# Optimization experiments

Measured on AMD Instinct MI355X. Metric: run time of the kernel, lower is better.

## Reference

```python
import jax, jax.numpy as jnp
import numpy as np

# ---- constants from module defaults ----
IMG, PS, STRIDE, C_IN = 224, 16, 8, 1
NP1D = (IMG - PS) // STRIDE + 1          # 27
NUM_PATCHES = NP1D * NP1D                # 729
EMBED = 64
N_INPUT = NUM_PATCHES * EMBED            # 46656
N_HIDDEN = 1000                          # d_model
N_RNN = 100
N_STEPS = 5
BETA, THR = 0.8, 0.5
BETA_R, THR_R = 0.95, 1.0
LM_SPN = 0.0058
ALPHA = 2.0  # snntorch ATan surrogate default

@jax.custom_vjp
def spike(x):
    return (x > 0).astype(x.dtype)

def _spike_fwd(x):
    return spike(x), x

def _spike_bwd(x, g):
    # snntorch ATan surrogate gradient
    return (g * (ALPHA / 2.0) / (1.0 + (jnp.pi / 2.0 * ALPHA * x) ** 2),)

spike.defvjp(_spike_fwd, _spike_bwd)

def extract_patches(x):
    # x: [B, C, H, W] -> [B, num_patches, C*PS*PS] matching torch unfold+permute+flatten
    B, C, H, W = x.shape
    idx = (jnp.arange(NP1D)[:, None] * STRIDE + jnp.arange(PS)).reshape(-1)  # [NP1D*PS]
    t = x[:, :, idx, :].reshape(B, C, NP1D, PS, W)
    t = t[..., idx].reshape(B, C, NP1D, PS, NP1D, PS)
    t = t.transpose(0, 2, 4, 1, 3, 5)  # [B, nh, nw, C, ph, pw]
    return t.reshape(B, NUM_PATCHES, C * PS * PS)

def setup_inputs() -> dict:
    key = jax.random.key(0)
    ks = jax.random.split(key, 12)
    def lin(k, fi, fo):
        kw, kb = jax.random.split(k)
        s = 1.0 / np.sqrt(fi)
        return (jax.random.uniform(kw, (fi, fo), jnp.float32, -s, s),
                jax.random.uniform(kb, (fo,), jnp.float32, -s, s))
    W_pe, b_pe = lin(ks[0], C_IN * PS * PS, EMBED)
    pos_embed = 0.02 * jax.random.normal(ks[1], (1, NUM_PATCHES, EMBED), jnp.float32)
    W1, b1 = lin(ks[2], N_INPUT, N_HIDDEN)
    W2, b2 = lin(ks[3], N_HIDDEN, N_HIDDEN)
    W3, b3 = lin(ks[4], N_HIDDEN, N_HIDDEN)
    WR, bR = lin(ks[5], N_HIDDEN, N_RNN)
    Vw, Vb = lin(ks[6], N_RNN, N_RNN)      # RLeaky recurrent linear
    Wq, bq = lin(ks[7], N_RNN, N_HIDDEN)
    Wk, bk = lin(ks[8], N_HIDDEN, N_HIDDEN)
    Wv, bv = lin(ks[9], N_HIDDEN, N_HIDDEN)
    Wo, bo = lin(ks[10], N_HIDDEN, 1)       # cross_last=True -> output_proj to 1
    data = jax.random.normal(ks[11], (32, C_IN, IMG, IMG), jnp.float32)
    return {"data": data, "W_pe": W_pe, "b_pe": b_pe, "pos_embed": pos_embed,
            "W1": W1, "b1": b1, "W2": W2, "b2": b2, "W3": W3, "b3": b3,
            "WR": WR, "bR": bR, "Vw": Vw, "Vb": Vb,
            "Wq": Wq, "bq": bq, "Wk": Wk, "bk": bk, "Wv": Wv, "bv": bv,
            "Wo": Wo, "bo": bo}

def _forward(data, W_pe, b_pe, pos_embed, W1, b1, W2, b2, W3, b3,
             WR, bR, Vw, Vb, Wq, bq, Wk, bk, Wv, bv, Wo, bo):
    B = data.shape[0]
    patches = extract_patches(data)                      # [B, 729, 256]
    x = patches @ W_pe + b_pe + pos_embed               # [B, 729, 64]
    x_flat = x.reshape(B, -1)                            # [B, 46656]
    cur1 = x_flat @ W1 + b1                              # constant across steps
    scale = jnp.sqrt(jnp.asarray(N_HIDDEN, jnp.float32))  # head_dim = d_model (1 head)

    def leaky(mem, cur, beta=BETA, thr=THR):
        reset = jax.lax.stop_gradient(spike(mem - thr))
        mem = beta * mem + cur - reset * thr
        return mem, spike(mem - thr)

    def step(carry, t):
        mem1, mem2, mem3, spk_r, mem_r, mem_out, total, prev, reg = carry
        # layers[:2] call -- first Leaky1 update
        mem1, spk1 = leaky(mem1, cur1)
        # layers[:7] call -- Leaky1 state updated a SECOND time (same x_flat)
        mem1, spk1b = leaky(mem1, cur1)
        mem2, spk2 = leaky(mem2, spk1b @ W2 + b2)
        mem3, spk3 = leaky(mem3, spk2 @ W3 + b3)  # Dropout is identity in eval
        total = total + spk1.mean() + spk3.mean()
        # RLeaky (beta=0.95, threshold=1.0, subtract reset, recurrent linear)
        rlin = spk1 @ WR + bR
        reset_r = jax.lax.stop_gradient(spike(mem_r - THR_R))
        mem_r = BETA_R * mem_r + rlin + spk_r @ Vw + Vb - reset_r * THR_R
        spk_r = spike(mem_r - THR_R)
        total = total + spk_r.mean()
        # cross-attention: feature dim acts as the sequence dim (seq=1 in view)
        q = spk_r @ Wq + bq                               # [B, 1000]
        k = spk3 @ Wk + bk                                # [B, 1000]
        v = spk3 @ Wv + bv                                # [B, 1000]
        probs = jax.nn.softmax(q[:, :, None] * k[:, None, :] / scale, axis=-1)  # [B,1000,1000]
        att = jnp.einsum('bij,bj->bi', probs, v) @ Wo + bo  # [B, 1]
        mem_out, spk_out = leaky(mem_out, att)
        mem_out = jax.lax.stop_gradient(mem_out)          # .detach() in source
        total = total + spk_out.mean()
        reg = reg + LM_SPN * total + jnp.where(t > 0, LM_SPN * jnp.abs(total - prev), 0.0)
        return (mem1, mem2, mem3, spk_r, mem_r, mem_out, total, total, reg), spk_out

    z = jnp.float32(0.0)
    init = (jnp.zeros((B, N_HIDDEN)), jnp.zeros((B, N_HIDDEN)), jnp.zeros((B, N_HIDDEN)),
            jnp.zeros((B, N_RNN)), jnp.zeros((B, N_RNN)), jnp.zeros((B, 1)), z, z, z)
    carry, spk_rec = jax.lax.scan(step, init, jnp.arange(N_STEPS))
    out = spk_rec.sum(0)[:, 0] / N_STEPS                  # [B]
    reg_norm = carry[-1] / N_STEPS
    return out, reg_norm

def reference(data, W_pe, b_pe, pos_embed, W1, b1, W2, b2, W3, b3,
              WR, bR, Vw, Vb, Wq, bq, Wk, bk, Wv, bv, Wo, bo):
    return _forward(data, W_pe, b_pe, pos_embed, W1, b1, W2, b2, W3, b3,
                    WR, bR, Vw, Vb, Wq, bq, Wk, bk, Wv, bv, Wo, bo)
```

## Files before the change

kernel.cpp:

```cpp
#include <hip/hip_runtime.h>

#define OFF_X     0
#define OFF_CUR1  1492992
#define OFF_MEM1  1524992
#define OFF_MEM2  1556992
#define OFF_MEM3  1588992
#define OFF_MEMR  1844992
#define OFF_SPKR  1848192
#define OFF_MEMO  1851392
#define OFF_PATT  1851424
#define OFF_CNT   1851680
#define OFF_OACC  1851700
#define OFF_SC    1851732
#define OFF_TICK  1851736
#define OFF_PART  1851744
#define OFF_PG2   OFF_PART
#define OFF_PG3   (OFF_PART + 800000)
#define OFF_PKK   (OFF_PART + 1600000)
#define OFF_PVV   (OFF_PART + 2400000)
#define OFF_M2B   (OFF_PART + 3200000)
#define OFF_M3B   (OFF_PART + 3232000)
#define OFF_M1B   (OFF_PART + 3264000)
#define OFF_SPK1  (OFF_PART + 3296000)
#define OFF_MRB   (OFF_PART + 3328000)
#define OFF_SRB   (OFF_PART + 3331200)

static constexpr float kBETA  = 0.8f;
static constexpr float kTHR   = 0.5f;
static constexpr float kBETAR = 0.95f;
static constexpr float kTHRR  = 1.0f;
static constexpr float kLM    = 0.0058f;

__global__ void k_init(float* ws) {
    int idx = blockIdx.x * 256 + threadIdx.x;
    if (idx < 96000) {
        ws[OFF_MEM1 + idx] = 0.f;
    } else {
        int j = idx - 96000;
        if (j < 6752) ws[OFF_MEMR + j] = 0.f;
    }
}

__global__ __launch_bounds__(64) void k_patch(
    const float* __restrict__ data, const float* __restrict__ Wpe,
    const float* __restrict__ bpe, const float* __restrict__ pos,
    float* __restrict__ xf)
{
    int b = blockIdx.x, pr = blockIdx.y;
    int tid = threadIdx.x;
    const float* db = data + (size_t)b * 50176 + pr * 1792;
    float bb = bpe[tid];
    float acc[27];
    #pragma unroll
    for (int pc = 0; pc < 27; ++pc)
        acc[pc] = bb + pos[(pr * 27 + pc) * 64 + tid];
    #pragma unroll 2
    for (int c = 0; c < 256; ++c) {
        float w = Wpe[c * 64 + tid];
        const float* row = db + (c >> 4) * 224 + (c & 15);
        #pragma unroll
        for (int pc = 0; pc < 27; ++pc)
            acc[pc] = fmaf(row[pc * 8], w, acc[pc]);
    }
    size_t obase = (size_t)b * 46656 + (size_t)pr * 27 * 64 + tid;
    #pragma unroll
    for (int pc = 0; pc < 27; ++pc)
        xf[obase + (size_t)pc * 64] = acc[pc];
}

__global__ __launch_bounds__(256) void k_gemm1_part(
    const float* __restrict__ xf, const float* __restrict__ W1,
    float* __restrict__ part, int tpc)
{
    int chunk = blockIdx.x;
    int hg = blockIdx.y;
    int t0 = chunk * tpc;
    int t1 = t0 + tpc; if (t1 > 729) t1 = 729;
    int tid = threadIdx.x;
    __shared__ float xs[2048];
    float acc[32][2];
    #pragma unroll
    for (int b = 0; b < 32; ++b) { acc[b][0] = 0.f; acc[b][1] = 0.f; }

    const int hbase = hg * 500;
    const bool ok1 = (tid + 256) < 500;
    const int h0 = hbase + tid;
    const int h1 = hbase + (ok1 ? tid + 256 : 0);
    for (int tt = t0; tt < t1; ++tt) {
        int i0 = tt * 64;
        __syncthreads();
        for (int l = tid; l < 2048; l += 256)
            xs[l] = xf[(size_t)(l >> 6) * 46656 + i0 + (l & 63)];
        __syncthreads();
        for (int ii4 = 0; ii4 < 16; ++ii4) {
            int i = i0 + ii4 * 4;
            const float* c0 = W1 + (size_t)i * 1000 + h0;
            const float* c1 = W1 + (size_t)i * 1000 + h1;
            float w0a = c0[0], w1a = c0[1000], w2a = c0[2000], w3a = c0[3000];
            float w0b = ok1 ? c1[0]    : 0.f;
            float w1b = ok1 ? c1[1000] : 0.f;
            float w2b = ok1 ? c1[2000] : 0.f;
            float w3b = ok1 ? c1[3000] : 0.f;
            #pragma unroll
            for (int b = 0; b < 32; ++b) {
                float4 xv = *reinterpret_cast<const float4*>(&xs[b * 64 + ii4 * 4]);
                float a0 = acc[b][0], a1 = acc[b][1];
                a0 = fmaf(xv.x, w0a, a0);  a1 = fmaf(xv.x, w0b, a1);
                a0 = fmaf(xv.y, w1a, a0);  a1 = fmaf(xv.y, w1b, a1);
                a0 = fmaf(xv.z, w2a, a0);  a1 = fmaf(xv.z, w2b, a1);
                a0 = fmaf(xv.w, w3a, a0);  a1 = fmaf(xv.w, w3b, a1);
                acc[b][0] = a0; acc[b][1] = a1;
            }
        }
    }
    float* pc = part + (size_t)chunk * 32000 + hbase;
    #pragma unroll
    for (int b = 0; b < 32; ++b) {
        pc[b * 1000 + tid] = acc[b][0];
        if (ok1) pc[b * 1000 + tid + 256] = acc[b][1];
    }
}

__global__ void k_gemm1_reduce(const float* __restrict__ part,
                               const float* __restrict__ b1,
                               float* __restrict__ cur1, int nchunk)
{
    int idx = blockIdx.x * 128 + threadIdx.x;
    if (idx >= 32000) return;
    int h = idx % 1000;
    float a0 = b1[h], a1 = 0.f, a2 = 0.f, a3 = 0.f;
    int c = 0;
    for (; c + 4 <= nchunk; c += 4) {
        a0 += part[(size_t)c * 32000 + idx];
        a1 += part[(size_t)(c + 1) * 32000 + idx];
        a2 += part[(size_t)(c + 2) * 32000 + idx];
        a3 += part[(size_t)(c + 3) * 32000 + idx];
    }
    for (; c < nchunk; ++c) a0 += part[(size_t)c * 32000 + idx];
    cur1[idx] = (a0 + a1) + (a2 + a3);
}

__global__ __launch_bounds__(256) void k_gsp(
    const float* __restrict__ cur1, const float* __restrict__ mem1_old,
    float* __restrict__ mem1_new, float* __restrict__ spk1_out,
    const float* __restrict__ W, float* __restrict__ part, float* cnt0)
{
    int hb = blockIdx.x, kc = blockIdx.y, bg = blockIdx.z;
    int tid = threadIdx.x;
    int j0 = kc * 40;
    __shared__ __align__(16) float al[320];
    __shared__ float redg[8 * 128];
    __shared__ float csum[4];
    float localc = 0.f;
    for (int e = tid; e < 320; e += 256) {
        int jj = e % 40, bi = e / 40;
        int idx = (bg * 8 + bi) * 1000 + j0 + jj;
        float m = mem1_old[idx], c = cur1[idx];
        float r1 = (m - kTHR > 0.f) ? kTHR : 0.f;
        float ma = __fsub_rn(__fadd_rn(__fmul_rn(kBETA, m), c), r1);
        float s1 = (ma - kTHR > 0.f) ? 1.f : 0.f;
        float r2 = __fmul_rn(s1, kTHR);
        float mb = __fsub_rn(__fadd_rn(__fmul_rn(kBETA, ma), c), r2);
        float s1b = (mb - kTHR > 0.f) ? 1.f : 0.f;
        al[jj * 8 + bi] = s1b;
        if (hb == 0) { mem1_new[idx] = mb; spk1_out[idx] = s1; localc += s1; }
    }
    for (int off = 32; off; off >>= 1) localc += __shfl_down(localc, off, 64);
    if ((tid & 63) == 0) csum[tid >> 6] = localc;
    __syncthreads();
    if (hb == 0 && tid == 0) {
        float tot = csum[0] + csum[1] + csum[2] + csum[3];
        if (tot != 0.f) atomicAdd(cnt0, tot);
    }
    int ks = tid >> 7, hh = tid & 127;
    float acc[8];
    #pragma unroll
    for (int b = 0; b < 8; ++b) acc[b] = 0.f;
    if (hh < 125) {
        int h = hb * 125 + hh;
        const float* Wp = W + (size_t)(j0 + ks * 20) * 1000 + h;
        const float4* abase = reinterpret_cast<const float4*>(&al[ks * 20 * 8]);
        #pragma unroll 4
        for (int jj = 0; jj < 20; ++jj) {
            float w = Wp[(size_t)jj * 1000];
            const float4* a4 = abase + jj * 2;
            #pragma unroll
            for (int q = 0; q < 2; ++q) {
                float4 av = a4[q];
                acc[q * 4 + 0] = fmaf(av.x, w, acc[q * 4 + 0]);
                acc[q * 4 + 1] = fmaf(av.y, w, acc[q * 4 + 1]);
                acc[q * 4 + 2] = fmaf(av.z, w, acc[q * 4 + 2]);
                acc[q * 4 + 3] = fmaf(av.w, w, acc[q * 4 + 3]);
            }
        }
    }
    if (ks == 1 && hh < 125) {
        #pragma unroll
        for (int b = 0; b < 8; ++b) redg[b * 128 + hh] = acc[b];
    }
    __syncthreads();
    if (ks == 0 && hh < 125) {
        int h = hb * 125 + hh;
        float* pp = part + (size_t)kc * 32000 + (size_t)(bg * 8) * 1000 + h;
        #pragma unroll
        for (int b = 0; b < 8; ++b) pp[(size_t)b * 1000] = acc[b] + redg[b * 128 + hh];
    }
}

template <bool COUNT>
__global__ __launch_bounds__(256) void k_gspred(
    const float* __restrict__ pin, const float* __restrict__ bias,
    const float* __restrict__ mem_old, float* __restrict__ mem_new,
    const float* __restrict__ W, float* __restrict__ pout, float* cnt)
{
    int hs = blockIdx.x, kc = blockIdx.y, bg = blockIdx.z;
    int tid = threadIdx.x;
    int j0 = kc * 40;
    __shared__ __align__(16) float al[320];
    __shared__ float redg[8 * 128];
    __shared__ float csum[4];
    float localc = 0.f;
    for (int e = tid; e < 320; e += 256) {
        int jj = e % 40, bi = e / 40;
        int idx = (bg * 8 + bi) * 1000 + j0 + jj;
        float a = bias[j0 + jj];
        #pragma unroll 5
        for (int c = 0; c < 25; ++c) a += pin[(size_t)c * 32000 + idx];
        float m = mem_old[idx];
        float r = (m - kTHR > 0.f) ? kTHR : 0.f;
        float mn = __fsub_rn(__fadd_rn(__fmul_rn(kBETA, m), a), r);
        float s = (mn - kTHR > 0.f) ? 1.f : 0.f;
        al[jj * 8 + bi] = s;
        if (hs == 0) { mem_new[idx] = mn; localc += s; }
    }
    if (COUNT) {
        for (int off = 32; off; off >>= 1) localc += __shfl_down(localc, off, 64);
        if ((tid & 63) == 0) csum[tid >> 6] = localc;
    }
    __syncthreads();
    if (COUNT && tid == 0 && hs == 0) {
        float tot = csum[0] + csum[1] + csum[2] + csum[3];
        if (tot != 0.f) atomicAdd(cnt, tot);
    }
    int ks = tid >> 7, hh = tid & 127;
    float acc[8];
    #pragma unroll
    for (int b = 0; b < 8; ++b) acc[b] = 0.f;
    if (hh < 125) {
        int h = hs * 125 + hh;
        const float* Wp = W + (size_t)(j0 + ks * 20) * 1000 + h;
        const float4* abase = reinterpret_cast<const float4*>(&al[ks * 20 * 8]);
        #pragma unroll 4
        for (int jj = 0; jj < 20; ++jj) {
            float w = Wp[(size_t)jj * 1000];
            const float4* a4 = abase + jj * 2;
            #pragma unroll
            for (int q = 0; q < 2; ++q) {
                float4 av = a4[q];
                acc[q * 4 + 0] = fmaf(av.x, w, acc[q * 4 + 0]);
                acc[q * 4 + 1] = fmaf(av.y, w, acc[q * 4 + 1]);
                acc[q * 4 + 2] = fmaf(av.z, w, acc[q * 4 + 2]);
                acc[q * 4 + 3] = fmaf(av.w, w, acc[q * 4 + 3]);
            }
        }
    }
    if (ks == 1 && hh < 125) {
        #pragma unroll
        for (int b = 0; b < 8; ++b) redg[b * 128 + hh] = acc[b];
    }
    __syncthreads();
    if (ks == 0 && hh < 125) {
        int h = hs * 125 + hh;
        float* pp = pout + (size_t)kc * 32000 + (size_t)(bg * 8) * 1000 + h;
        #pragma unroll
        for (int b = 0; b < 8; ++b) pp[(size_t)b * 1000] = acc[b] + redg[b * 128 + hh];
    }
}

__global__ __launch_bounds__(256) void k_gspred_kv(
    const float* __restrict__ pin, const float* __restrict__ bias,
    const float* __restrict__ mem_old, float* __restrict__ mem_new,
    const float* __restrict__ Wk, const float* __restrict__ Wv,
    float* __restrict__ pk, float* __restrict__ pv, float* cnt)
{
    int hs = blockIdx.x, kc = blockIdx.y, bg = blockIdx.z;
    int tid = threadIdx.x;
    int j0 = kc * 40;
    __shared__ __align__(16) float al[320];
    __shared__ float redk[8 * 128];
    __shared__ float redv[8 * 128];
    __shared__ float csum[4];
    float localc = 0.f;
    for (int e = tid; e < 320; e += 256) {
        int jj = e % 40, bi = e / 40;
        int idx = (bg * 8 + bi) * 1000 + j0 + jj;
        float a = bias[j0 + jj];
        #pragma unroll 5
        for (int c = 0; c < 25; ++c) a += pin[(size_t)c * 32000 + idx];
        float m = mem_old[idx];
        float r = (m - kTHR > 0.f) ? kTHR : 0.f;
        float mn = __fsub_rn(__fadd_rn(__fmul_rn(kBETA, m), a), r);
        float s = (mn - kTHR > 0.f) ? 1.f : 0.f;
        al[jj * 8 + bi] = s;
        if (hs == 0) { mem_new[idx] = mn; localc += s; }
    }
    for (int off = 32; off; off >>= 1) localc += __shfl_down(localc, off, 64);
    if ((tid & 63) == 0) csum[tid >> 6] = localc;
    __syncthreads();
    if (tid == 0 && hs == 0) {
        float tot = csum[0] + csum[1] + csum[2] + csum[3];
        if (tot != 0.f) atomicAdd(cnt, tot);
    }
    int ks = tid >> 7, hh = tid & 127;
    float ak[8], av2[8];
    #pragma unroll
    for (int b = 0; b < 8; ++b) { ak[b] = 0.f; av2[b] = 0.f; }
    if (hh < 125) {
        int h = hs * 125 + hh;
        const float* wkp = Wk + (size_t)(j0 + ks * 20) * 1000 + h;
        const float* wvp = Wv + (size_t)(j0 + ks * 20) * 1000 + h;
        const float4* abase = reinterpret_cast<const float4*>(&al[ks * 20 * 8]);
        #pragma unroll 4
        for (int jj = 0; jj < 20; ++jj) {
            float wk = wkp[(size_t)jj * 1000];
            float wv = wvp[(size_t)jj * 1000];
            const float4* a4 = abase + jj * 2;
            #pragma unroll
            for (int q = 0; q < 2; ++q) {
                float4 av = a4[q];
                ak[q * 4 + 0] = fmaf(av.x, wk, ak[q * 4 + 0]);
                ak[q * 4 + 1] = fmaf(av.y, wk, ak[q * 4 + 1]);
                ak[q * 4 + 2] = fmaf(av.z, wk, ak[q * 4 + 2]);
                ak[q * 4 + 3] = fmaf(av.w, wk, ak[q * 4 + 3]);
                av2[q * 4 + 0] = fmaf(av.x, wv, av2[q * 4 + 0]);
                av2[q * 4 + 1] = fmaf(av.y, wv, av2[q * 4 + 1]);
                av2[q * 4 + 2] = fmaf(av.z, wv, av2[q * 4 + 2]);
                av2[q * 4 + 3] = fmaf(av.w, wv, av2[q * 4 + 3]);
            }
        }
    }
    if (ks == 1 && hh < 125) {
        #pragma unroll
        for (int b = 0; b < 8; ++b) { redk[b * 128 + hh] = ak[b]; redv[b * 128 + hh] = av2[b]; }
    }
    __syncthreads();
    if (ks == 0 && hh < 125) {
        int h = hs * 125 + hh;
        float* ppk = pk + (size_t)kc * 32000 + (size_t)(bg * 8) * 1000 + h;
        float* ppv = pv + (size_t)kc * 32000 + (size_t)(bg * 8) * 1000 + h;
        #pragma unroll
        for (int b = 0; b < 8; ++b) {
            ppk[(size_t)b * 1000] = ak[b] + redk[b * 128 + hh];
            ppv[(size_t)b * 1000] = av2[b] + redv[b * 128 + hh];
        }
    }
}

__global__ __launch_bounds__(512) void k_attnred(
    const float* __restrict__ pkk, const float* __restrict__ pvv,
    const float* __restrict__ bk, const float* __restrict__ bv,
    const float* __restrict__ spk1, const float* __restrict__ WR,
    const float* __restrict__ bR, const float* __restrict__ Vw,
    const float* __restrict__ Vb,
    const float* __restrict__ memr_old, float* __restrict__ memr_new,
    const float* __restrict__ spkr_old, float* __restrict__ spkr_new,
    const float* __restrict__ Wq, const float* __restrict__ bq,
    const float* __restrict__ Wo, const float* __restrict__ bo,
    float* __restrict__ patt, float* __restrict__ memo,
    float* __restrict__ oacc, const float* __restrict__ cnt,
    float* __restrict__ sc, float* __restrict__ dout,
    unsigned int* __restrict__ tick, float* cnt2, int t)
{
    int it = blockIdx.x, b = blockIdx.y;
    int tid = threadIdx.x;
    __shared__ float kk[1000], vv[1000];
    __shared__ float sr[100];
    __shared__ float s1l[1000];
    __shared__ float red2[512];
    __shared__ float red[512];
    __shared__ float pden[512], pnum[512];
    __shared__ int isLast;

    for (int l = tid; l < 1000; l += 512) s1l[l] = spk1[b * 1000 + l];
    if (tid < 100) sr[tid] = spkr_old[b * 100 + tid];
    __syncthreads();
    int ks4 = tid >> 7, hh4 = tid & 127;
    float p = 0.f;
    if (hh4 < 100) {
        const float* wp = WR + (size_t)(ks4 * 250) * 100 + hh4;
        int j0r = ks4 * 250;
        #pragma unroll 5
        for (int j = 0; j < 250; ++j) p = fmaf(s1l[j0r + j], wp[(size_t)j * 100], p);
    }
    red2[ks4 * 128 + hh4] = p;
    __syncthreads();
    float snew = 0.f;
    if (tid < 100) {
        float acc = bR[tid] + ((red2[tid] + red2[128 + tid]) + (red2[256 + tid] + red2[384 + tid]));
        float rec = 0.f;
        for (int j = 0; j < 100; ++j) rec = fmaf(sr[j], Vw[j * 100 + tid], rec);
        float m = memr_old[b * 100 + tid];
        float r = (m - kTHRR > 0.f) ? kTHRR : 0.f;
        float mn = __fsub_rn(__fadd_rn(__fadd_rn(__fadd_rn(__fmul_rn(kBETAR, m), acc), rec), Vb[tid]), r);
        snew = (mn - kTHRR > 0.f) ? 1.f : 0.f;
        if (it == 0) { memr_new[b * 100 + tid] = mn; spkr_new[b * 100 + tid] = snew; }
    }
    if (it == 0) {
        unsigned long long mskr = __ballot(snew > 0.5f);
        if ((tid & 63) == 0) {
            int pc2 = __popcll(mskr);
            if (pc2) atomicAdd(cnt2, (float)pc2);
        }
    }
    __syncthreads();
    if (tid < 100) sr[tid] = snew;
    __syncthreads();

    float pmax = -3.4e38f, pmin = 3.4e38f;
    for (int h = tid; h < 1000; h += 512) {
        int idx = b * 1000 + h;
        float ak = bk[h], av = bv[h];
        #pragma unroll 5
        for (int c = 0; c < 25; ++c) {
            ak += pkk[(size_t)c * 32000 + idx];
            av += pvv[(size_t)c * 32000 + idx];
        }
        kk[h] = ak; vv[h] = av;
        pmax = fmaxf(pmax, ak);
        pmin = fminf(pmin, ak);
    }
    red[tid] = pmax;
    __syncthreads();
    for (int s2 = 256; s2 > 0; s2 >>= 1) {
        if (tid < s2) red[tid] = fmaxf(red[tid], red[tid + s2]);
        __syncthreads();
    }
    float kmax = red[0];
    __syncthreads();
    red[tid] = pmin;
    __syncthreads();
    for (int s2 = 256; s2 > 0; s2 >>= 1) {
        if (tid < s2) red[tid] = fminf(red[tid], red[tid + s2]);
        __syncthreads();
    }
    float kmin = red[0];
    __syncthreads();

    int quarter = tid >> 7, lane = tid & 127;
    float den = 0.f, num = 0.f;
    if (lane < 125) {
        int i = it * 125 + lane;
        float qi = bq[i];
        for (int j = 0; j < 100; ++j) qi = fmaf(sr[j], Wq[j * 1000 + i], qi);
        float qs = qi / 31.62277660168379f;
        float m = (qs >= 0.f) ? qs * kmax : qs * kmin;
        int jb = quarter * 250;
        for (int j = 0; j < 250; ++j) {
            float e = __expf(fmaf(qs, kk[jb + j], -m));
            den += e;
            num = fmaf(e, vv[jb + j], num);
        }
    }
    pden[tid] = den; pnum[tid] = num;
    __syncthreads();
    float pw = 0.f;
    if (tid < 125) {
        float dsum = (pden[tid] + pden[tid + 128]) + (pden[tid + 256] + pden[tid + 384]);
        float nsum = (pnum[tid] + pnum[tid + 128]) + (pnum[tid + 256] + pnum[tid + 384]);
        pw = (nsum / dsum) * Wo[it * 125 + tid];
    }
    red[tid] = (tid < 125) ? pw : 0.f;
    __syncthreads();
    for (int s2 = 256; s2 > 0; s2 >>= 1) {
        if (tid < s2) red[tid] += red[tid + s2];
        __syncthreads();
    }
    if (tid == 0) patt[b * 8 + it] = red[0];
    __syncthreads();
    if (tid == 0) {
        __threadfence();
        unsigned r = atomicAdd(tick, 1u);
        isLast = (r == 255u) ? 1 : 0;
    }
    __syncthreads();
    if (isLast && tid < 64) {
        __threadfence();
        float s = 0.f;
        if (tid < 32) {
            float a = bo[0];
            for (int itx = 0; itx < 8; ++itx) a += patt[tid * 8 + itx];
            float m = memo[tid];
            float r = (m - kTHR > 0.f) ? kTHR : 0.f;
            float mn = __fsub_rn(__fadd_rn(__fmul_rn(kBETA, m), a), r);
            memo[tid] = mn;
            s = (mn - kTHR > 0.f) ? 1.f : 0.f;
            float oa = oacc[tid] + s;
            oacc[tid] = oa;
            if (t == 4) dout[tid] = oa / 5.0f;
        }
        unsigned long long msk = __ballot(s > 0.5f);
        float co = (float)__popcll(msk);
        if (tid == 0) {
            float total = sc[0];
            float prev = total;
            total = __fadd_rn(total, __fdiv_rn(cnt[0], 32000.f));
            total = __fadd_rn(total, __fdiv_rn(cnt[1], 32000.f));
            total = __fadd_rn(total, __fdiv_rn(cnt[2], 3200.f));
            total = __fadd_rn(total, __fdiv_rn(co, 32.f));
            float reg = sc[1];
            reg = __fadd_rn(reg, __fmul_rn(kLM, total));
            if (t > 0) reg = __fadd_rn(reg, __fmul_rn(kLM, fabsf(__fsub_rn(total, prev))));
            sc[0] = total; sc[1] = reg;
            if (t == 4) dout[32] = reg / 5.0f;
        }
    }
}

extern "C" void kernel_launch(void* const* d_in, const int* in_sizes, int n_in,
                              void* d_out, int out_size, void* d_ws, size_t ws_size,
                              hipStream_t stream)
{
    const float* data = (const float*)d_in[0];
    const float* Wpe  = (const float*)d_in[1];
    const float* bpe  = (const float*)d_in[2];
    const float* pos  = (const float*)d_in[3];
    const float* W1   = (const float*)d_in[4];
    const float* b1   = (const float*)d_in[5];
    const float* W2   = (const float*)d_in[6];
    const float* b2   = (const float*)d_in[7];
    const float* W3   = (const float*)d_in[8];
    const float* b3   = (const float*)d_in[9];
    const float* WR   = (const float*)d_in[10];
    const float* bR   = (const float*)d_in[11];
    const float* Vw   = (const float*)d_in[12];
    const float* Vb   = (const float*)d_in[13];
    const float* Wq   = (const float*)d_in[14];
    const float* bq   = (const float*)d_in[15];
    const float* Wk   = (const float*)d_in[16];
    const float* bk   = (const float*)d_in[17];
    const float* Wv   = (const float*)d_in[18];
    const float* bv   = (const float*)d_in[19];
    const float* Wo   = (const float*)d_in[20];
    const float* bo   = (const float*)d_in[21];

    float* ws = (float*)d_ws;
    float* dout = (float*)d_out;

    float* xf    = ws + OFF_X;
    float* cur1  = ws + OFF_CUR1;
    float* mem1a = ws + OFF_MEM1;
    float* mem2a = ws + OFF_MEM2;
    float* mem3a = ws + OFF_MEM3;
    float* memra = ws + OFF_MEMR;
    float* spkra = ws + OFF_SPKR;
    float* memo  = ws + OFF_MEMO;
    float* patt  = ws + OFF_PATT;
    float* cntb  = ws + OFF_CNT;
    float* oacc  = ws + OFF_OACC;
    float* sc    = ws + OFF_SC;
    unsigned int* tick = (unsigned int*)(ws + OFF_TICK);
    float* part  = ws + OFF_PART;
    float* pg2   = ws + OFF_PG2;
    float* pg3   = ws + OFF_PG3;
    float* pkk   = ws + OFF_PKK;
    float* pvv   = ws + OFF_PVV;
    float* mem2b = ws + OFF_M2B;
    float* mem3b = ws + OFF_M3B;
    float* mem1b = ws + OFF_M1B;
    float* spk1  = ws + OFF_SPK1;
    float* memrb = ws + OFF_MRB;
    float* spkrb = ws + OFF_SRB;

    size_t ws_f = ws_size / 4;
    size_t avail = (ws_f > OFF_PART) ? (ws_f - OFF_PART) : 0;
    long nchunk_l = (long)(avail / 32000);
    int nchunk = (nchunk_l > 365) ? 365 : (int)nchunk_l;
    if (nchunk < 1) nchunk = 1;
    int tpc = (729 + nchunk - 1) / nchunk;
    nchunk = (729 + tpc - 1) / tpc;

    k_init<<<402, 256, 0, stream>>>(ws);
    k_patch<<<dim3(32, 27), 64, 0, stream>>>(data, Wpe, bpe, pos, xf);
    k_gemm1_part<<<dim3(nchunk, 2), 256, 0, stream>>>(xf, W1, part, tpc);
    k_gemm1_reduce<<<250, 128, 0, stream>>>(part, b1, cur1, nchunk);

    for (int t = 0; t < 5; ++t) {
        float* cnt = cntb + t * 4;
        float* m1o = (t & 1) ? mem1b : mem1a;
        float* m1n = (t & 1) ? mem1a : mem1b;
        float* m2o = (t & 1) ? mem2b : mem2a;
        float* m2n = (t & 1) ? mem2a : mem2b;
        float* m3o = (t & 1) ? mem3b : mem3a;
        float* m3n = (t & 1) ? mem3a : mem3b;
        float* mro = (t & 1) ? memrb : memra;
        float* mrn = (t & 1) ? memra : memrb;
        float* sro = (t & 1) ? spkrb : spkra;
        float* srn = (t & 1) ? spkra : spkrb;

        k_gsp<<<dim3(8, 25, 4), 256, 0, stream>>>(
            cur1, m1o, m1n, spk1, W2, pg2, cnt + 0);
        k_gspred<false><<<dim3(8, 25, 4), 256, 0, stream>>>(
            pg2, b2, m2o, m2n, W3, pg3, nullptr);
        k_gspred_kv<<<dim3(8, 25, 4), 256, 0, stream>>>(
            pg3, b3, m3o, m3n, Wk, Wv, pkk, pvv, cnt + 1);
        k_attnred<<<dim3(8, 32), 512, 0, stream>>>(
            pkk, pvv, bk, bv, spk1, WR, bR, Vw, Vb,
            mro, mrn, sro, srn, Wq, bq, Wo, bo,
            patt, memo, oacc, cnt, sc, dout, tick + t, cnt + 2, t);
    }
    (void)in_sizes; (void)n_in; (void)out_size;
}
```

Baseline: 517.7 us.

## Halve batch per block in spiking GEMVs, widen reductions, use wave shuffles

The per-step spiking GEMV kernels now process 4 batch rows per block instead of 8, doubling the grid's z-dimension to put more blocks in flight. The gemm1 reduce kernel unrolls 8 accumulators. The chunk cap for gemm1 partials rises from 365 to 729, so partials can be split further when workspace allows. The attention kernel replaces shared-memory tree reductions with wave shuffles plus a small cross-wave combine. Together these aim to raise occupancy and cut synchronisation, at the cost of re-reading each weight twice as often and possibly more partial-sum traffic.

```diff
diff --git a/kernel.cpp b/kernel.cpp
--- a/kernel.cpp
+++ b/kernel.cpp
@@ -129,15 +129,20 @@
     if (idx >= 32000) return;
     int h = idx % 1000;
     float a0 = b1[h], a1 = 0.f, a2 = 0.f, a3 = 0.f;
+    float a4 = 0.f, a5 = 0.f, a6 = 0.f, a7 = 0.f;
     int c = 0;
-    for (; c + 4 <= nchunk; c += 4) {
+    for (; c + 8 <= nchunk; c += 8) {
         a0 += part[(size_t)c * 32000 + idx];
         a1 += part[(size_t)(c + 1) * 32000 + idx];
         a2 += part[(size_t)(c + 2) * 32000 + idx];
         a3 += part[(size_t)(c + 3) * 32000 + idx];
+        a4 += part[(size_t)(c + 4) * 32000 + idx];
+        a5 += part[(size_t)(c + 5) * 32000 + idx];
+        a6 += part[(size_t)(c + 6) * 32000 + idx];
+        a7 += part[(size_t)(c + 7) * 32000 + idx];
     }
     for (; c < nchunk; ++c) a0 += part[(size_t)c * 32000 + idx];
-    cur1[idx] = (a0 + a1) + (a2 + a3);
+    cur1[idx] = ((a0 + a1) + (a2 + a3)) + ((a4 + a5) + (a6 + a7));
 }
 
 __global__ __launch_bounds__(256) void k_gsp(
@@ -148,13 +153,13 @@
     int hb = blockIdx.x, kc = blockIdx.y, bg = blockIdx.z;
     int tid = threadIdx.x;
     int j0 = kc * 40;
-    __shared__ __align__(16) float al[320];
-    __shared__ float redg[8 * 128];
+    __shared__ __align__(16) float al[160];
+    __shared__ float redg[4 * 128];
     __shared__ float csum[4];
     float localc = 0.f;
-    for (int e = tid; e < 320; e += 256) {
-        int jj = e % 40, bi = e / 40;
-        int idx = (bg * 8 + bi) * 1000 + j0 + jj;
+    if (tid < 160) {
+        int jj = tid % 40, bi = tid / 40;
+        int idx = (bg * 4 + bi) * 1000 + j0 + jj;
         float m = mem1_old[idx], c = cur1[idx];
         float r1 = (m - kTHR > 0.f) ? kTHR : 0.f;
         float ma = __fsub_rn(__fadd_rn(__fmul_rn(kBETA, m), c), r1);
@@ -162,8 +167,8 @@
         float r2 = __fmul_rn(s1, kTHR);
         float mb = __fsub_rn(__fadd_rn(__fmul_rn(kBETA, ma), c), r2);
         float s1b = (mb - kTHR > 0.f) ? 1.f : 0.f;
-        al[jj * 8 + bi] = s1b;
-        if (hb == 0) { mem1_new[idx] = mb; spk1_out[idx] = s1; localc += s1; }
+        al[jj * 4 + bi] = s1b;
+        if (hb == 0) { mem1_new[idx] = mb; spk1_out[idx] = s1; localc = s1; }
     }
     for (int off = 32; off; off >>= 1) localc += __shfl_down(localc, off, 64);
     if ((tid & 63) == 0) csum[tid >> 6] = localc;
@@ -173,37 +178,31 @@
         if (tot != 0.f) atomicAdd(cnt0, tot);
     }
     int ks = tid >> 7, hh = tid & 127;
-    float acc[8];
-    #pragma unroll
-    for (int b = 0; b < 8; ++b) acc[b] = 0.f;
+    float acc[4] = {0.f, 0.f, 0.f, 0.f};
     if (hh < 125) {
         int h = hb * 125 + hh;
         const float* Wp = W + (size_t)(j0 + ks * 20) * 1000 + h;
-        const float4* abase = reinterpret_cast<const float4*>(&al[ks * 20 * 8]);
+        const float4* abase = reinterpret_cast<const float4*>(&al[ks * 20 * 4]);
         #pragma unroll 4
         for (int jj = 0; jj < 20; ++jj) {
             float w = Wp[(size_t)jj * 1000];
-            const float4* a4 = abase + jj * 2;
-            #pragma unroll
-            for (int q = 0; q < 2; ++q) {
-                float4 av = a4[q];
-                acc[q * 4 + 0] = fmaf(av.x, w, acc[q * 4 + 0]);
-                acc[q * 4 + 1] = fmaf(av.y, w, acc[q * 4 + 1]);
-                acc[q * 4 + 2] = fmaf(av.z, w, acc[q * 4 + 2]);
-                acc[q * 4 + 3] = fmaf(av.w, w, acc[q * 4 + 3]);
-            }
+            float4 av = abase[jj];
+            acc[0] = fmaf(av.x, w, acc[0]);
+            acc[1] = fmaf(av.y, w, acc[1]);
+            acc[2] = fmaf(av.z, w, acc[2]);
+            acc[3] = fmaf(av.w, w, acc[3]);
         }
     }
     if (ks == 1 && hh < 125) {
         #pragma unroll
-        for (int b = 0; b < 8; ++b) redg[b * 128 + hh] = acc[b];
+        for (int b = 0; b < 4; ++b) redg[b * 128 + hh] = acc[b];
     }
     __syncthreads();
     if (ks == 0 && hh < 125) {
         int h = hb * 125 + hh;
-        float* pp = part + (size_t)kc * 32000 + (size_t)(bg * 8) * 1000 + h;
-        #pragma unroll
-        for (int b = 0; b < 8; ++b) pp[(size_t)b * 1000] = acc[b] + redg[b * 128 + hh];
+        float* pp = part + (size_t)kc * 32000 + (size_t)(bg * 4) * 1000 + h;
+        #pragma unroll
+        for (int b = 0; b < 4; ++b) pp[(size_t)b * 1000] = acc[b] + redg[b * 128 + hh];
     }
 }
 
@@ -216,13 +215,13 @@
     int hs = blockIdx.x, kc = blockIdx.y, bg = blockIdx.z;
     int tid = threadIdx.x;
     int j0 = kc * 40;
-    __shared__ __align__(16) float al[320];
-    __shared__ float redg[8 * 128];
+    __shared__ __align__(16) float al[160];
+    __shared__ float redg[4 * 128];
     __shared__ float csum[4];
     float localc = 0.f;
-    for (int e = tid; e < 320; e += 256) {
-        int jj = e % 40, bi = e / 40;
-        int idx = (bg * 8 + bi) * 1000 + j0 + jj;
+    if (tid < 160) {
+        int jj = tid % 40, bi = tid / 40;
+        int idx = (bg * 4 + bi) * 1000 + j0 + jj;
         float a = bias[j0 + jj];
         #pragma unroll 5
         for (int c = 0; c < 25; ++c) a += pin[(size_t)c * 32000 + idx];
@@ -230,8 +229,8 @@
         float r = (m - kTHR > 0.f) ? kTHR : 0.f;
         float mn = __fsub_rn(__fadd_rn(__fmul_rn(kBETA, m), a), r);
         float s = (mn - kTHR > 0.f) ? 1.f : 0.f;
-        al[jj * 8 + bi] = s;
-        if (hs == 0) { mem_new[idx] = mn; localc += s; }
+        al[jj * 4 + bi] = s;
+        if (hs == 0) { mem_new[idx] = mn; localc = s; }
     }
     if (COUNT) {
         for (int off = 32; off; off >>= 1) localc += __shfl_down(localc, off, 64);
@@ -243,37 +242,31 @@
         if (tot != 0.f) atomicAdd(cnt, tot);
     }
     int ks = tid >> 7, hh = tid & 127;
-    float acc[8];
-    #pragma unroll
-    for (int b = 0; b < 8; ++b) acc[b] = 0.f;
+    float acc[4] = {0.f, 0.f, 0.f, 0.f};
     if (hh < 125) {
         int h = hs * 125 + hh;
         const float* Wp = W + (size_t)(j0 + ks * 20) * 1000 + h;
-        const float4* abase = reinterpret_cast<const float4*>(&al[ks * 20 * 8]);
+        const float4* abase = reinterpret_cast<const float4*>(&al[ks * 20 * 4]);
         #pragma unroll 4
         for (int jj = 0; jj < 20; ++jj) {
             float w = Wp[(size_t)jj * 1000];
-            const float4* a4 = abase + jj * 2;
-            #pragma unroll
-            for (int q = 0; q < 2; ++q) {
-                float4 av = a4[q];
-                acc[q * 4 + 0] = fmaf(av.x, w, acc[q * 4 + 0]);
-                acc[q * 4 + 1] = fmaf(av.y, w, acc[q * 4 + 1]);
-                acc[q * 4 + 2] = fmaf(av.z, w, acc[q * 4 + 2]);
-                acc[q * 4 + 3] = fmaf(av.w, w, acc[q * 4 + 3]);
-            }
+            float4 av = abase[jj];
+            acc[0] = fmaf(av.x, w, acc[0]);
+            acc[1] = fmaf(av.y, w, acc[1]);
+            acc[2] = fmaf(av.z, w, acc[2]);
+            acc[3] = fmaf(av.w, w, acc[3]);
         }
     }
     if (ks == 1 && hh < 125) {
         #pragma unroll
-        for (int b = 0; b < 8; ++b) redg[b * 128 + hh] = acc[b];
+        for (int b = 0; b < 4; ++b) redg[b * 128 + hh] = acc[b];
     }
     __syncthreads();
     if (ks == 0 && hh < 125) {
         int h = hs * 125 + hh;
-        float* pp = pout + (size_t)kc * 32000 + (size_t)(bg * 8) * 1000 + h;
-        #pragma unroll
-        for (int b = 0; b < 8; ++b) pp[(size_t)b * 1000] = acc[b] + redg[b * 128 + hh];
+        float* pp = pout + (size_t)kc * 32000 + (size_t)(bg * 4) * 1000 + h;
+        #pragma unroll
+        for (int b = 0; b < 4; ++b) pp[(size_t)b * 1000] = acc[b] + redg[b * 128 + hh];
     }
 }
 
@@ -286,14 +279,14 @@
     int hs = blockIdx.x, kc = blockIdx.y, bg = blockIdx.z;
     int tid = threadIdx.x;
     int j0 = kc * 40;
-    __shared__ __align__(16) float al[320];
-    __shared__ float redk[8 * 128];
-    __shared__ float redv[8 * 128];
+    __shared__ __align__(16) float al[160];
+    __shared__ float redk[4 * 128];
+    __shared__ float redv[4 * 128];
     __shared__ float csum[4];
     float localc = 0.f;
-    for (int e = tid; e < 320; e += 256) {
-        int jj = e % 40, bi = e / 40;
-        int idx = (bg * 8 + bi) * 1000 + j0 + jj;
+    if (tid < 160) {
+        int jj = tid % 40, bi = tid / 40;
+        int idx = (bg * 4 + bi) * 1000 + j0 + jj;
         float a = bias[j0 + jj];
         #pragma unroll 5
         for (int c = 0; c < 25; ++c) a += pin[(size_t)c * 32000 + idx];
@@ -301,8 +294,8 @@
         float r = (m - kTHR > 0.f) ? kTHR : 0.f;
         float mn = __fsub_rn(__fadd_rn(__fmul_rn(kBETA, m), a), r);
         float s = (mn - kTHR > 0.f) ? 1.f : 0.f;
-        al[jj * 8 + bi] = s;
-        if (hs == 0) { mem_new[idx] = mn; localc += s; }
+        al[jj * 4 + bi] = s;
+        if (hs == 0) { mem_new[idx] = mn; localc = s; }
     }
     for (int off = 32; off; off >>= 1) localc += __shfl_down(localc, off, 64);
     if ((tid & 63) == 0) csum[tid >> 6] = localc;
@@ -312,44 +305,35 @@
         if (tot != 0.f) atomicAdd(cnt, tot);
     }
     int ks = tid >> 7, hh = tid & 127;
-    float ak[8], av2[8];
-    #pragma unroll
-    for (int b = 0; b < 8; ++b) { ak[b] = 0.f; av2[b] = 0.f; }
+    float ak[4] = {0.f, 0.f, 0.f, 0.f};
+    float av2[4] = {0.f, 0.f, 0.f, 0.f};
     if (hh < 125) {
         int h = hs * 125 + hh;
         const float* wkp = Wk + (size_t)(j0 + ks * 20) * 1000 + h;
         const float* wvp = Wv + (size_t)(j0 + ks * 20) * 1000 + h;
-        const float4* abase = reinterpret_cast<const float4*>(&al[ks * 20 * 8]);
+        const float4* abase = reinterpret_cast<const float4*>(&al[ks * 20 * 4]);
         #pragma unroll 4
         for (int jj = 0; jj < 20; ++jj) {
             float wk = wkp[(size_t)jj * 1000];
             float wv = wvp[(size_t)jj * 1000];
-            const float4* a4 = abase + jj * 2;
-            #pragma unroll
-            for (int q = 0; q < 2; ++q) {
-                float4 av = a4[q];
-                ak[q * 4 + 0] = fmaf(av.x, wk, ak[q * 4 + 0]);
-                ak[q * 4 + 1] = fmaf(av.y, wk, ak[q * 4 + 1]);
-                ak[q * 4 + 2] = fmaf(av.z, wk, ak[q * 4 + 2]);
-                ak[q * 4 + 3] = fmaf(av.w, wk, ak[q * 4 + 3]);
-                av2[q * 4 + 0] = fmaf(av.x, wv, av2[q * 4 + 0]);
-                av2[q * 4 + 1] = fmaf(av.y, wv, av2[q * 4 + 1]);
-                av2[q * 4 + 2] = fmaf(av.z, wv, av2[q * 4 + 2]);
-                av2[q * 4 + 3] = fmaf(av.w, wv, av2[q * 4 + 3]);
-            }
+            float4 av = abase[jj];
+            ak[0] = fmaf(av.x, wk, ak[0]);  av2[0] = fmaf(av.x, wv, av2[0]);
+            ak[1] = fmaf(av.y, wk, ak[1]);  av2[1] = fmaf(av.y, wv, av2[1]);
+            ak[2] = fmaf(av.z, wk, ak[2]);  av2[2] = fmaf(av.z, wv, av2[2]);
+            ak[3] = fmaf(av.w, wk, ak[3]);  av2[3] = fmaf(av.w, wv, av2[3]);
         }
     }
     if (ks == 1 && hh < 125) {
         #pragma unroll
-        for (int b = 0; b < 8; ++b) { redk[b * 128 + hh] = ak[b]; redv[b * 128 + hh] = av2[b]; }
+        for (int b = 0; b < 4; ++b) { redk[b * 128 + hh] = ak[b]; redv[b * 128 + hh] = av2[b]; }
     }
     __syncthreads();
     if (ks == 0 && hh < 125) {
         int h = hs * 125 + hh;
-        float* ppk = pk + (size_t)kc * 32000 + (size_t)(bg * 8) * 1000 + h;
-        float* ppv = pv + (size_t)kc * 32000 + (size_t)(bg * 8) * 1000 + h;
-        #pragma unroll
-        for (int b = 0; b < 8; ++b) {
+        float* ppk = pk + (size_t)kc * 32000 + (size_t)(bg * 4) * 1000 + h;
+        float* ppv = pv + (size_t)kc * 32000 + (size_t)(bg * 4) * 1000 + h;
+        #pragma unroll
+        for (int b = 0; b < 4; ++b) {
             ppk[(size_t)b * 1000] = ak[b] + redk[b * 128 + hh];
             ppv[(size_t)b * 1000] = av2[b] + redv[b * 128 + hh];
         }
@@ -377,8 +361,8 @@
     __shared__ float sr[100];
     __shared__ float s1l[1000];
     __shared__ float red2[512];
-    __shared__ float red[512];
     __shared__ float pden[512], pnum[512];
+    __shared__ float wred[8], wred2[8];
     __shared__ int isLast;
 
     for (int l = tid; l < 1000; l += 512) s1l[l] = spk1[b * 1000 + l];
@@ -429,22 +413,18 @@
         pmax = fmaxf(pmax, ak);
         pmin = fminf(pmin, ak);
     }
-    red[tid] = pmax;
-    __syncthreads();
-    for (int s2 = 256; s2 > 0; s2 >>= 1) {
-        if (tid < s2) red[tid] = fmaxf(red[tid], red[tid + s2]);
-        __syncthreads();
-    }
-    float kmax = red[0];
-    __syncthreads();
-    red[tid] = pmin;
-    __syncthreads();
-    for (int s2 = 256; s2 > 0; s2 >>= 1) {
-        if (tid < s2) red[tid] = fminf(red[tid], red[tid + s2]);
-        __syncthreads();
-    }
-    float kmin = red[0];
-    __syncthreads();
+    for (int off = 32; off; off >>= 1) {
+        pmax = fmaxf(pmax, __shfl_down(pmax, off, 64));
+        pmin = fminf(pmin, __shfl_down(pmin, off, 64));
+    }
+    if ((tid & 63) == 0) { wred[tid >> 6] = pmax; wred2[tid >> 6] = pmin; }
+    __syncthreads();
+    float kmax = wred[0], kmin = wred2[0];
+    #pragma unroll
+    for (int w = 1; w < 8; ++w) {
+        kmax = fmaxf(kmax, wred[w]);
+        kmin = fminf(kmin, wred2[w]);
+    }
 
     int quarter = tid >> 7, lane = tid & 127;
     float den = 0.f, num = 0.f;
@@ -469,13 +449,14 @@
         float nsum = (pnum[tid] + pnum[tid + 128]) + (pnum[tid + 256] + pnum[tid + 384]);
         pw = (nsum / dsum) * Wo[it * 125 + tid];
     }
-    red[tid] = (tid < 125) ? pw : 0.f;
-    __syncthreads();
-    for (int s2 = 256; s2 > 0; s2 >>= 1) {
-        if (tid < s2) red[tid] += red[tid + s2];
-        __syncthreads();
-    }
-    if (tid == 0) patt[b * 8 + it] = red[0];
+    for (int off = 32; off; off >>= 1) pw += __shfl_down(pw, off, 64);
+    if ((tid & 63) == 0) wred[tid >> 6] = pw;
+    __syncthreads();
+    if (tid == 0) {
+        float tot = ((wred[0] + wred[1]) + (wred[2] + wred[3]))
+                  + ((wred[4] + wred[5]) + (wred[6] + wred[7]));
+        patt[b * 8 + it] = tot;
+    }
     __syncthreads();
     if (tid == 0) {
         __threadfence();
@@ -574,7 +555,7 @@
     size_t ws_f = ws_size / 4;
     size_t avail = (ws_f > OFF_PART) ? (ws_f - OFF_PART) : 0;
     long nchunk_l = (long)(avail / 32000);
-    int nchunk = (nchunk_l > 365) ? 365 : (int)nchunk_l;
+    int nchunk = (nchunk_l > 729) ? 729 : (int)nchunk_l;
     if (nchunk < 1) nchunk = 1;
     int tpc = (729 + nchunk - 1) / nchunk;
     nchunk = (729 + tpc - 1) / tpc;
@@ -597,11 +578,11 @@
         float* sro = (t & 1) ? spkrb : spkra;
         float* srn = (t & 1) ? spkra : spkrb;
 
-        k_gsp<<<dim3(8, 25, 4), 256, 0, stream>>>(
+        k_gsp<<<dim3(8, 25, 8), 256, 0, stream>>>(
             cur1, m1o, m1n, spk1, W2, pg2, cnt + 0);
-        k_gspred<false><<<dim3(8, 25, 4), 256, 0, stream>>>(
+        k_gspred<false><<<dim3(8, 25, 8), 256, 0, stream>>>(
             pg2, b2, m2o, m2n, W3, pg3, nullptr);
-        k_gspred_kv<<<dim3(8, 25, 4), 256, 0, stream>>>(
+        k_gspred_kv<<<dim3(8, 25, 8), 256, 0, stream>>>(
             pg3, b3, m3o, m3n, Wk, Wv, pkk, pvv, cnt + 1);
         k_attnred<<<dim3(8, 32), 512, 0, stream>>>(
             pkk, pvv, bk, bv, spk1, WR, bR, Vw, Vb,
```

Result: slower. 530.7 us (+2.5%).
